# Performance work log

Measured on AMD Instinct MI355X. Metric: run time of the kernel, lower is better.

The kernel has to match this reference:

```python
import jax, jax.numpy as jnp
import numpy as np

NUM_NODES = 20000
NUM_EDGES = 1_000_000
NUM_REL = 12        # internal num_relation (init arg 24 // 2)
NUM_STEP = 6
HID = 128
B_SET = 64          # number of unique (h, r) queries
BS, NEG = 64, 32    # scoring batch
EPS = 1e-10


def setup_inputs() -> dict:
    key = jax.random.key(0)
    ks = jax.random.split(key, 16)
    s = 0.1
    inp = {
        "query_emb": jax.random.normal(ks[0], (2 * NUM_REL + 1, HID), jnp.float32) * s,
        "w_ih": jax.random.normal(ks[1], (4 * HID, HID), jnp.float32) * s,
        "w_hh": jax.random.normal(ks[2], (4 * HID, HID), jnp.float32) * s,
        "b_ih": jax.random.normal(ks[3], (4 * HID,), jnp.float32) * s,
        "b_hh": jax.random.normal(ks[4], (4 * HID,), jnp.float32) * s,
        "wl_w": jax.random.normal(ks[5], (2 * NUM_REL, HID), jnp.float32) * s,
        "wl_b": jax.random.normal(ks[6], (2 * NUM_REL,), jnp.float32) * s,
        "lin_w": jax.random.normal(ks[7], (1, 1), jnp.float32),
        "lin_b": jax.random.normal(ks[8], (1,), jnp.float32),
        "edge_index": jax.random.randint(ks[9], (2, NUM_EDGES), 0, NUM_NODES, jnp.int64),
        "edge_type": jax.random.randint(ks[10], (NUM_EDGES,), 0, 2 * NUM_REL, jnp.int64),
        "h_set": jax.random.randint(ks[11], (B_SET,), 0, NUM_NODES, jnp.int64),
        "r_set": jax.random.randint(ks[12], (B_SET,), 0, NUM_REL, jnp.int64),
        "t_index": jax.random.randint(ks[13], (BS, NEG), 0, NUM_NODES, jnp.int64),
        "hr_inverse": jax.random.randint(ks[14], (BS, NEG), 0, B_SET, jnp.int64),
    }
    return inp


def _lstm(query, w_ih, w_hh, b_ih, b_hh):
    # query: [T, B, D]; single-layer PyTorch LSTM (gate order i, f, g, o)
    B, D = query.shape[1], w_hh.shape[1]
    h0 = jnp.zeros((B, D), query.dtype)

    def step(carry, x):
        h, c = carry
        gates = x @ w_ih.T + b_ih + h @ w_hh.T + b_hh
        i, f, g, o = jnp.split(gates, 4, axis=-1)
        c = jax.nn.sigmoid(f) * c + jax.nn.sigmoid(i) * jnp.tanh(g)
        h = jax.nn.sigmoid(o) * jnp.tanh(c)
        return (h, c), h

    _, hidden = jax.lax.scan(step, (h0, h0), query)
    return hidden  # [T, B, D]


def reference(query_emb, w_ih, w_hh, b_ih, b_hh, wl_w, wl_b, lin_w, lin_b,
              edge_index, edge_type, h_set, r_set, t_index, hr_inverse):
    N1 = NUM_NODES + 1
    B = h_set.shape[0]
    # query sequence: relation repeated (T-1) times, then END token (= NUM_REL)
    q_index = jnp.concatenate(
        [jnp.tile(r_set[None, :], (NUM_STEP - 1, 1)),
         jnp.full((1, B), NUM_REL, dtype=r_set.dtype)], axis=0)  # [T, B]
    query = query_emb[q_index]                                   # [T, B, D]
    hidden = _lstm(query, w_ih, w_hh, b_ih, b_hh)                # [T, B, D]

    memory = jax.nn.one_hot(h_set, N1, dtype=query_emb.dtype)[None]  # [1, B, N1]
    node_in, node_out = edge_index[0], edge_index[1]

    output = None
    for i in range(NUM_STEP):
        k = hidden[i]                 # [B, D]
        v = hidden[: i + 1]           # [i+1, B, D]
        attn = jax.nn.softmax(jnp.einsum('bd,tbd->bt', k, v), axis=-1)
        inp = jnp.einsum('bt,tbn->nb', attn, memory)             # [N1, B]
        weight = jax.nn.softmax(k @ wl_w.T + wl_b, axis=-1).T    # [2R, B]
        # gather -> weight -> scatter_add over edges (edge_weight == 1)
        message = inp[node_in] * weight[edge_type]               # [E, B]
        output = jax.ops.segment_sum(message, node_out, num_segments=N1)
        output = output / jnp.maximum(output.sum(0, keepdims=True), EPS)
        memory = jnp.concatenate([memory, output.T[None]], axis=0)

    score = output[t_index, hr_inverse]           # [BS, NEG]
    return score * lin_w[0, 0] + lin_b[0]
```

## Files before the change

kernel.cpp:

```cpp
#include <hip/hip_runtime.h>
#include <hip/hip_fp16.h>
#include <math.h>

namespace {

constexpr int kN1 = 20001;
constexpr int kNE = 1000000;
constexpr int kNStep = 6;
constexpr int kHid = 128;
constexpr int kB = 64;
constexpr int kNRel2 = 24;
constexpr float kEps = 1e-10f;
constexpr unsigned kSent = (unsigned)kN1;
constexpr int kPMax = kNE + 8 * kN1;
constexpr int kGatherBlocks = 2048;
constexpr int kNWaves = kGatherBlocks * 4;

__device__ __forceinline__ float sig(float x) { return 1.0f / (1.0f + expf(-x)); }

__device__ __forceinline__ float2 cvt2(unsigned u) {
  __half2 h = *reinterpret_cast<__half2*>(&u);
  return __half22float2(h);
}


__global__ __launch_bounds__(256) void transpose_w_kernel(
    const float* __restrict__ w_ih, const float* __restrict__ w_hh,
    float* __restrict__ wt) {
  const int idx = blockIdx.x * 256 + threadIdx.x;
  if (idx < 256 * 512) {
    const int k = idx >> 9;
    const int j = idx & 511;
    wt[idx] = (k < 128) ? w_ih[j * kHid + k] : w_hh[j * kHid + (k - 128)];
  }
}

__global__ __launch_bounds__(512) void lstm_fast_kernel(
    const float* __restrict__ query_emb, const float* __restrict__ wt,
    const float* __restrict__ b_ih, const float* __restrict__ b_hh,
    const int* __restrict__ r_set, float* __restrict__ hidden ) {
  const int b = blockIdx.x;
  const int tid = threadIdx.x;
  __shared__ float xh[256];
  __shared__ float cst[kHid];
  __shared__ float gsm[512];
  const float bias = b_ih[tid] + b_hh[tid];
  const int q = r_set[b];
  if (tid < kHid) { cst[tid] = 0.f; xh[kHid + tid] = 0.f; }
  for (int s = 0; s < kNStep; ++s) {
    if (tid < kHid) xh[tid] = query_emb[((s < kNStep - 1) ? q : 12) * kHid + tid];
    __syncthreads();
    float acc = bias;
#pragma unroll 8
    for (int k = 0; k < 256; ++k) acc += xh[k] * wt[k * 512 + tid];
    gsm[tid] = acc;
    __syncthreads();
    if (tid < kHid) {
      const float ig = sig(gsm[tid]);
      const float fg = sig(gsm[kHid + tid]);
      const float gg = tanhf(gsm[2 * kHid + tid]);
      const float og = sig(gsm[3 * kHid + tid]);
      const float cn = fg * cst[tid] + ig * gg;
      cst[tid] = cn;
      const float hn = og * tanhf(cn);
      xh[kHid + tid] = hn;
      hidden[(s * kB + b) * kHid + tid] = hn;
    }
    __syncthreads();
  }
}

__global__ __launch_bounds__(256) void lstm_kernel(
    const float* __restrict__ query_emb, const float* __restrict__ w_ih,
    const float* __restrict__ w_hh, const float* __restrict__ b_ih,
    const float* __restrict__ b_hh, const int* __restrict__ r_set,
    float* __restrict__ hidden) {
  const int b = blockIdx.x;
  const int tid = threadIdx.x;
  __shared__ float xs[kHid], hs[kHid], cs[kHid], gates[4 * kHid];
  if (tid < kHid) { hs[tid] = 0.f; cs[tid] = 0.f; }
  __syncthreads();
  for (int s = 0; s < kNStep; ++s) {
    const int q = (s < kNStep - 1) ? r_set[b] : 12;
    if (tid < kHid) xs[tid] = query_emb[q * kHid + tid];
    __syncthreads();
    for (int j = tid; j < 4 * kHid; j += blockDim.x) {
      const float* wi = &w_ih[j * kHid];
      const float* wh = &w_hh[j * kHid];
      float a = b_ih[j] + b_hh[j];
#pragma unroll 4
      for (int k = 0; k < kHid; ++k) a += xs[k] * wi[k] + hs[k] * wh[k];
      gates[j] = a;
    }
    __syncthreads();
    if (tid < kHid) {
      const float ig = sig(gates[tid]);
      const float fg = sig(gates[kHid + tid]);
      const float gg = tanhf(gates[2 * kHid + tid]);
      const float og = sig(gates[3 * kHid + tid]);
      const float cn = fg * cs[tid] + ig * gg;
      const float hn = og * tanhf(cn);
      cs[tid] = cn;
      hs[tid] = hn;
      hidden[(s * kB + b) * kHid + tid] = hn;
    }
    __syncthreads();
  }
}

__global__ __launch_bounds__(128) void attn_weight_kernel(
    const float* __restrict__ hidden, const float* __restrict__ wl_w,
    const float* __restrict__ wl_b, float* __restrict__ attnAll ,
    float* __restrict__ weightAll ) {
  const int b = blockIdx.x;
  const int tid = threadIdx.x;
  __shared__ float hsm[kNStep][kHid];
  __shared__ float G[kNStep][kNStep];
  __shared__ float logits[kNStep][kNRel2];
  for (int s = 0; s < kNStep; ++s) hsm[s][tid] = hidden[(s * kB + b) * kHid + tid];
  __syncthreads();
  if (tid < 36) {
    const int i = tid / 6, t = tid % 6;
    if (t <= i) {
      float acc = 0.f;
      for (int k = 0; k < kHid; ++k) acc += hsm[i][k] * hsm[t][k];
      G[i][t] = acc;
    }
  }
  for (int p = tid; p < kNStep * kNRel2; p += 128) {
    const int i = p / kNRel2, r = p % kNRel2;
    float acc = wl_b[r];
    for (int k = 0; k < kHid; ++k) acc += hsm[i][k] * wl_w[r * kHid + k];
    logits[i][r] = acc;
  }
  __syncthreads();
  if (tid < kNStep) {
    const int i = tid;
    float m = G[i][0];
    for (int t = 1; t <= i; ++t) m = fmaxf(m, G[i][t]);
    float ssum = 0.f;
    float ev[kNStep];
    for (int t = 0; t <= i; ++t) { ev[t] = expf(G[i][t] - m); ssum += ev[t]; }
    for (int t = 0; t <= i; ++t) attnAll[(i * kNStep + t) * kB + b] = ev[t] / ssum;
    float mw = logits[i][0];
    for (int r = 1; r < kNRel2; ++r) mw = fmaxf(mw, logits[i][r]);
    float sw = 0.f;
    float ew[kNRel2];
    for (int r = 0; r < kNRel2; ++r) { ew[r] = expf(logits[i][r] - mw); sw += ew[r]; }
    for (int r = 0; r < kNRel2; ++r) weightAll[(i * kNRel2 + r) * kB + b] = ew[r] / sw;
  }
}


__global__ __launch_bounds__(256) void zero_kernel(int* __restrict__ counts,
                                                   float* __restrict__ colsumAll) {
  const int i = blockIdx.x * blockDim.x + threadIdx.x;
  if (i < kN1) counts[i] = 0;
  if (i < kNStep * kB) colsumAll[i] = 0.f;
}

__global__ __launch_bounds__(256) void hist_kernel(const int* __restrict__ nout,
                                                   int* __restrict__ counts) {
  for (int e = blockIdx.x * blockDim.x + threadIdx.x; e < kNE;
       e += gridDim.x * blockDim.x)
    atomicAdd(&counts[nout[e]], 1);
}

__global__ __launch_bounds__(1024) void scan_kernel(const int* __restrict__ counts,
                                                    int* __restrict__ poffsets,
                                                    int* __restrict__ cursor) {
  __shared__ int part[1024];
  const int tid = threadIdx.x;
  const int chunk = (kN1 + 1023) / 1024;
  const int beg = tid * chunk;
  const int end = min(beg + chunk, kN1);
  int s = 0;
  for (int i = beg; i < end; ++i) s += (counts[i] + 7) & ~7;
  part[tid] = s;
  __syncthreads();
  for (int off = 1; off < 1024; off <<= 1) {
    const int v = (tid >= off) ? part[tid - off] : 0;
    __syncthreads();
    part[tid] += v;
    __syncthreads();
  }
  int run = part[tid] - s;
  for (int i = beg; i < end; ++i) {
    poffsets[i] = run;
    cursor[i] = run;
    run += (counts[i] + 7) & ~7;
  }
  if (tid == 1023) poffsets[kN1] = part[1023];
}

__global__ __launch_bounds__(256) void fill_kernel(unsigned* __restrict__ packed) {
  for (int i = blockIdx.x * blockDim.x + threadIdx.x; i < kPMax;
       i += gridDim.x * blockDim.x)
    packed[i] = kSent;
}

__global__ __launch_bounds__(256) void permute_kernel(
    const int* __restrict__ nin, const int* __restrict__ nout,
    const int* __restrict__ etype, int* __restrict__ cursor,
    unsigned* __restrict__ packed) {
  for (int e = blockIdx.x * blockDim.x + threadIdx.x; e < kNE;
       e += gridDim.x * blockDim.x) {
    const int d = nout[e];
    const int pos = atomicAdd(&cursor[d], 1);
    packed[pos] = (unsigned)nin[e] | ((unsigned)etype[e] << 15);
  }
}


__global__ __launch_bounds__(256) void inp_kernel(
    const float* __restrict__ attnAll, const float* __restrict__ colsumAll,
    const int* __restrict__ h_set, const float* __restrict__ outs,
    __half* __restrict__ inp, int step) {
  __shared__ float coef[kNStep][kB];
  __shared__ int hsm[kB];
  const int tid = threadIdx.x;
  for (int j = tid; j < kNStep * kB; j += 256) {
    const int t = j >> 6, b = j & 63;
    float c = 0.f;
    if (t == 0)
      c = attnAll[(step * kNStep) * kB + b];
    else if (t <= step)
      c = attnAll[(step * kNStep + t) * kB + b] /
          fmaxf(colsumAll[(t - 1) * kB + b], kEps);
    coef[t][b] = c;
  }
  if (tid < kB) hsm[tid] = h_set[tid];
  __syncthreads();
  const int total = (kN1 + 1) * 16;
  for (int idx = blockIdx.x * blockDim.x + tid; idx < total;
       idx += gridDim.x * blockDim.x) {
    const int n = idx >> 4;
    const int cg = idx & 15;
    float ax = 0.f, ay = 0.f, az = 0.f, aw = 0.f;
    if (n < kN1) {
      for (int t = 1; t <= step; ++t) {
        const float4 ct = *reinterpret_cast<const float4*>(&coef[t][cg * 4]);
        const float4 o = *reinterpret_cast<const float4*>(
            &outs[((long long)(t - 1) * kN1 + n) * kB + cg * 4]);
        ax += ct.x * o.x; ay += ct.y * o.y; az += ct.z * o.z; aw += ct.w * o.w;
      }
      const int c0 = cg * 4;
      if (hsm[c0 + 0] == n) ax += coef[0][c0 + 0];
      if (hsm[c0 + 1] == n) ay += coef[0][c0 + 1];
      if (hsm[c0 + 2] == n) az += coef[0][c0 + 2];
      if (hsm[c0 + 3] == n) aw += coef[0][c0 + 3];
    }
    __half2 h0 = __floats2half2_rn(ax, ay);
    __half2 h1 = __floats2half2_rn(az, aw);
    uint2 u;
    u.x = *reinterpret_cast<unsigned*>(&h0);
    u.y = *reinterpret_cast<unsigned*>(&h1);
    *reinterpret_cast<uint2*>(inp + (long long)idx * 4) = u;
  }
}

__global__ __launch_bounds__(256) void gather_seg_kernel(
    const __half* __restrict__ inp ,
    const float* __restrict__ weight ,
    const unsigned* __restrict__ packed, const int* __restrict__ poffsets,
    float* __restrict__ out, float* __restrict__ colsum) {
  __shared__ __align__(16) __half wsm[kNRel2 * kB];
  __shared__ float red[4][kB];
  const int tid = threadIdx.x;
  const int lane = tid & 63;
  const int wid = tid >> 6;
  const int g = lane >> 3;
  const int cb = lane & 7;
  for (int j = tid; j < kNRel2 * kB; j += 256) wsm[j] = __float2half(weight[j]);
  __syncthreads();

  float csum[8] = {0.f, 0.f, 0.f, 0.f, 0.f, 0.f, 0.f, 0.f};
  float acc[8] = {0.f, 0.f, 0.f, 0.f, 0.f, 0.f, 0.f, 0.f};

  auto flushNode = [&](int node) {
#pragma unroll
    for (int j = 0; j < 8; ++j) {
      acc[j] += __shfl_xor(acc[j], 8);
      acc[j] += __shfl_xor(acc[j], 16);
      acc[j] += __shfl_xor(acc[j], 32);
    }
    if (g == 0) {
      *reinterpret_cast<float4*>(out + (long long)node * kB + cb * 8) =
          make_float4(acc[0], acc[1], acc[2], acc[3]);
      *reinterpret_cast<float4*>(out + (long long)node * kB + cb * 8 + 4) =
          make_float4(acc[4], acc[5], acc[6], acc[7]);
#pragma unroll
      for (int j = 0; j < 8; ++j) csum[j] += acc[j];
    }
#pragma unroll
    for (int j = 0; j < 8; ++j) acc[j] = 0.f;
  };

  const int wave = blockIdx.x * 4 + wid;
  const int P = poffsets[kN1];
  const int nG = P >> 3;
  const int chunkG = (nG + kNWaves - 1) / kNWaves;
  const int gbeg = wave * chunkG;
  if (gbeg < nG) {
    const int gend = min(gbeg + chunkG, nG);
    auto lb = [&](int x) {
      int lo = 0, hi = kN1;
      while (lo < hi) {
        const int mid = (lo + hi) >> 1;
        if (poffsets[mid] < x) lo = mid + 1; else hi = mid;
      }
      return lo;
    };
    const int nbeg = lb(gbeg * 8);
    const int nend = (gend >= nG) ? kN1 : lb(gend * 8);
    if (nbeg < nend) {
      int n = nbeg;
      int nextB = poffsets[n + 1];
      const int ebeg = poffsets[nbeg];
      const int eend = poffsets[nend];
      unsigned pA = (ebeg < eend) ? packed[ebeg + g] : kSent;
      unsigned pB = (ebeg + 8 < eend) ? packed[ebeg + 8 + g] : kSent;
      uint4 vA = *reinterpret_cast<const uint4*>(
          inp + (long long)(pA & 0x7fffu) * kB + cb * 8);
      uint4 vB = *reinterpret_cast<const uint4*>(
          inp + (long long)(pB & 0x7fffu) * kB + cb * 8);
      for (int ebase = ebeg; ebase < eend; ebase += 16) {
        const bool hasB = (ebase + 8) < eend;
        const int e2 = ebase + 16, e3 = ebase + 24;
        const unsigned pC = (e2 < eend) ? packed[e2 + g] : kSent;
        const unsigned pD = (e3 < eend) ? packed[e3 + g] : kSent;
        while (ebase >= nextB) { flushNode(n); ++n; nextB = poffsets[n + 1]; }
        {
          const uint4 w4 =
              *reinterpret_cast<const uint4*>(wsm + (pA >> 15) * kB + cb * 8);
          const float2 v0 = cvt2(vA.x), v1 = cvt2(vA.y), v2 = cvt2(vA.z), v3 = cvt2(vA.w);
          const float2 w0 = cvt2(w4.x), w1 = cvt2(w4.y), w2 = cvt2(w4.z), w3 = cvt2(w4.w);
          acc[0] += v0.x * w0.x; acc[1] += v0.y * w0.y;
          acc[2] += v1.x * w1.x; acc[3] += v1.y * w1.y;
          acc[4] += v2.x * w2.x; acc[5] += v2.y * w2.y;
          acc[6] += v3.x * w3.x; acc[7] += v3.y * w3.y;
        }
        if (hasB) {
          while (ebase + 8 >= nextB) { flushNode(n); ++n; nextB = poffsets[n + 1]; }
          const uint4 w4 =
              *reinterpret_cast<const uint4*>(wsm + (pB >> 15) * kB + cb * 8);
          const float2 v0 = cvt2(vB.x), v1 = cvt2(vB.y), v2 = cvt2(vB.z), v3 = cvt2(vB.w);
          const float2 w0 = cvt2(w4.x), w1 = cvt2(w4.y), w2 = cvt2(w4.z), w3 = cvt2(w4.w);
          acc[0] += v0.x * w0.x; acc[1] += v0.y * w0.y;
          acc[2] += v1.x * w1.x; acc[3] += v1.y * w1.y;
          acc[4] += v2.x * w2.x; acc[5] += v2.y * w2.y;
          acc[6] += v3.x * w3.x; acc[7] += v3.y * w3.y;
        }
        pA = pC; pB = pD;
        vA = *reinterpret_cast<const uint4*>(
            inp + (long long)(pC & 0x7fffu) * kB + cb * 8);
        vB = *reinterpret_cast<const uint4*>(
            inp + (long long)(pD & 0x7fffu) * kB + cb * 8);
      }
      while (n < nend) { flushNode(n); ++n; }
    }
  }
  if (g == 0) {
#pragma unroll
    for (int j = 0; j < 8; ++j) red[wid][cb * 8 + j] = csum[j];
  }
  __syncthreads();
  if (wid == 0) {
    const float r = red[0][lane] + red[1][lane] + red[2][lane] + red[3][lane];
    unsafeAtomicAdd(&colsum[lane], r);
  }
}

__global__ __launch_bounds__(256) void score_kernel(
    const float* __restrict__ outLast, const float* __restrict__ colsumLast,
    const int* __restrict__ t_index, const int* __restrict__ hr_inverse,
    const float* __restrict__ lin_w, const float* __restrict__ lin_b,
    float* __restrict__ out, int n) {
  const int i = blockIdx.x * blockDim.x + threadIdx.x;
  if (i < n) {
    const int node = t_index[i];
    const int b = hr_inverse[i];
    const float v = outLast[(long long)node * kB + b] / fmaxf(colsumLast[b], kEps);
    out[i] = v * lin_w[0] + lin_b[0];
  }
}


__global__ __launch_bounds__(256) void inp_zero_kernel(
    const float* __restrict__ attnAll, const int* __restrict__ h_set,
    const float* __restrict__ outs, float* __restrict__ inp,
    float* __restrict__ out_next, float* __restrict__ colsum, int step) {
  const long long total = (long long)kN1 * kB;
  for (long long idx = (long long)blockIdx.x * blockDim.x + threadIdx.x; idx < total;
       idx += (long long)gridDim.x * blockDim.x) {
    const int b = (int)(idx & 63);
    const int n = (int)(idx >> 6);
    float acc = (h_set[b] == n) ? attnAll[(step * kNStep) * kB + b] : 0.f;
    for (int t = 1; t <= step; ++t)
      acc += attnAll[(step * kNStep + t) * kB + b] *
             outs[(long long)(t - 1) * kN1 * kB + idx];
    inp[idx] = acc;
    out_next[idx] = 0.f;
  }
  if (blockIdx.x == 0 && threadIdx.x < kB) colsum[threadIdx.x] = 0.f;
}

__global__ __launch_bounds__(256) void scatter_kernel(
    const float* __restrict__ inp, const float* __restrict__ weight,
    const int* __restrict__ nin, const int* __restrict__ nout,
    const int* __restrict__ etype, float* __restrict__ out,
    float* __restrict__ colsum) {
  const int lane = threadIdx.x & 63;
  const int wave = blockIdx.x * (blockDim.x >> 6) + (threadIdx.x >> 6);
  const int nwave = gridDim.x * (blockDim.x >> 6);
  __shared__ float wsm[kNRel2 * kB];
  for (int j = threadIdx.x; j < kNRel2 * kB; j += blockDim.x) wsm[j] = weight[j];
  __syncthreads();
  float csum = 0.f;
  for (int e = wave; e < kNE; e += nwave) {
    const float v = inp[(long long)nin[e] * kB + lane] * wsm[etype[e] * kB + lane];
    unsafeAtomicAdd(&out[(long long)nout[e] * kB + lane], v);
    csum += v;
  }
  unsafeAtomicAdd(&colsum[lane], csum);
}

__global__ __launch_bounds__(256) void normalize_kernel(
    float* __restrict__ out, const float* __restrict__ colsum) {
  const long long total = (long long)kN1 * kB;
  for (long long idx = (long long)blockIdx.x * blockDim.x + threadIdx.x; idx < total;
       idx += (long long)gridDim.x * blockDim.x)
    out[idx] /= fmaxf(colsum[idx & 63], kEps);
}

__global__ __launch_bounds__(256) void score_kernel_norm(
    const float* __restrict__ outLast, const int* __restrict__ t_index,
    const int* __restrict__ hr_inverse, const float* __restrict__ lin_w,
    const float* __restrict__ lin_b, float* __restrict__ out, int n) {
  const int i = blockIdx.x * blockDim.x + threadIdx.x;
  if (i < n) {
    out[i] = outLast[(long long)t_index[i] * kB + hr_inverse[i]] * lin_w[0] + lin_b[0];
  }
}

}

extern "C" void kernel_launch(void* const* d_in, const int* in_sizes, int n_in,
                              void* d_out, int out_size, void* d_ws, size_t ws_size,
                              hipStream_t stream) {
  const float* query_emb = (const float*)d_in[0];
  const float* w_ih = (const float*)d_in[1];
  const float* w_hh = (const float*)d_in[2];
  const float* b_ih = (const float*)d_in[3];
  const float* b_hh = (const float*)d_in[4];
  const float* wl_w = (const float*)d_in[5];
  const float* wl_b = (const float*)d_in[6];
  const float* lin_w = (const float*)d_in[7];
  const float* lin_b = (const float*)d_in[8];
  const int* edge_index = (const int*)d_in[9];
  const int* edge_type = (const int*)d_in[10];
  const int* h_set = (const int*)d_in[11];
  const int* r_set = (const int*)d_in[12];
  const int* t_index = (const int*)d_in[13];
  const int* hr_inverse = (const int*)d_in[14];
  float* out = (float*)d_out;

  const int* nin = edge_index;
  const int* nout = edge_index + kNE;

  float* ws = (float*)d_ws;
  float* hidden = ws;
  float* attnAll = hidden + kNStep * kB * kHid;
  float* weightAll = attnAll + kNStep * kNStep * kB;
  float* colsumAll = weightAll + kNStep * kNRel2 * kB;
  float* inpF32 = colsumAll + kNStep * kB;
  __half* inpH = (__half*)inpF32;
  float* outs = inpF32 + (long long)kN1 * kB;
  float* tail = outs + (long long)kNStep * kN1 * kB;
  int* counts = (int*)tail;
  int* poffsets = counts + kN1;
  int* cursor = poffsets + kN1 + 1;
  unsigned* packed = (unsigned*)(cursor + kN1);
  float* wt = (float*)(packed + kPMax);
  const size_t needed = (size_t)((char*)(wt + 256 * 512) - (char*)d_ws);

  if (ws_size >= needed) {
    transpose_w_kernel<<<512, 256, 0, stream>>>(w_ih, w_hh, wt);
    lstm_fast_kernel<<<kB, 512, 0, stream>>>(query_emb, wt, b_ih, b_hh, r_set, hidden);
    attn_weight_kernel<<<kB, 128, 0, stream>>>(hidden, wl_w, wl_b, attnAll, weightAll);

    zero_kernel<<<(kN1 + 255) / 256, 256, 0, stream>>>(counts, colsumAll);
    hist_kernel<<<1024, 256, 0, stream>>>(nout, counts);
    scan_kernel<<<1, 1024, 0, stream>>>(counts, poffsets, cursor);
    fill_kernel<<<1024, 256, 0, stream>>>(packed);
    permute_kernel<<<1024, 256, 0, stream>>>(nin, nout, edge_type, cursor, packed);

    const int inp_threads = (kN1 + 1) * 16;
    for (int i = 0; i < kNStep; ++i) {
      float* out_i = outs + (long long)i * kN1 * kB;
      inp_kernel<<<(inp_threads + 255) / 256, 256, 0, stream>>>(
          attnAll, colsumAll, h_set, outs, inpH, i);
      gather_seg_kernel<<<kGatherBlocks, 256, 0, stream>>>(
          inpH, weightAll + i * kNRel2 * kB, packed, poffsets, out_i,
          colsumAll + i * kB);
    }
    score_kernel<<<(out_size + 255) / 256, 256, 0, stream>>>(
        outs + 5LL * kN1 * kB, colsumAll + 5 * kB, t_index, hr_inverse, lin_w, lin_b,
        out, out_size);
  } else {
    lstm_kernel<<<kB, 256, 0, stream>>>(query_emb, w_ih, w_hh, b_ih, b_hh, r_set,
                                        hidden);
    attn_weight_kernel<<<kB, 128, 0, stream>>>(hidden, wl_w, wl_b, attnAll, weightAll);
    float* colsum = colsumAll;
    for (int i = 0; i < kNStep; ++i) {
      float* out_i = outs + (long long)i * kN1 * kB;
      inp_zero_kernel<<<2048, 256, 0, stream>>>(attnAll, h_set, outs, inpF32, out_i,
                                                colsum, i);
      scatter_kernel<<<4096, 256, 0, stream>>>(inpF32, weightAll + i * kNRel2 * kB,
                                               nin, nout, edge_type, out_i, colsum);
      normalize_kernel<<<2048, 256, 0, stream>>>(out_i, colsum);
    }
    score_kernel_norm<<<(out_size + 255) / 256, 256, 0, stream>>>(
        outs + 5LL * kN1 * kB, t_index, hr_inverse, lin_w, lin_b, out, out_size);
  }
}
```

Baseline: 669.7 us.

## Replace destination-sorted CSR gather with partitioned source-sorted atomic scatter

Edges are no longer sorted by destination node. They are bucketed into 8 destination partitions and sorted by source inside each partition, using per-XCD histograms and a three-kernel multi-block scan. The step kernel now scatters with float atomics into the output, reusing the source's inp value across consecutive edges. Zeroing of the next output is folded into the inp kernel. This removes the single-block scan, the padding fill and the per-node segment handling, but adds atomic contention on outputs and an extra memory pass. It also stores the count arrays in the outs buffer region, relying on that space being free during preprocessing.

```diff
diff --git a/kernel.cpp b/kernel.cpp
--- a/kernel.cpp
+++ b/kernel.cpp
@@ -4,6 +4,7 @@
 
 namespace {
 
+constexpr int kNN = 20000;
 constexpr int kN1 = 20001;
 constexpr int kNE = 1000000;
 constexpr int kNStep = 6;
@@ -11,17 +12,15 @@
 constexpr int kB = 64;
 constexpr int kNRel2 = 24;
 constexpr float kEps = 1e-10f;
-constexpr unsigned kSent = (unsigned)kN1;
-constexpr int kPMax = kNE + 8 * kN1;
-constexpr int kGatherBlocks = 2048;
-constexpr int kNWaves = kGatherBlocks * 4;
+constexpr int kNXcd = 8;
+constexpr int kPart = 8;
+constexpr int kPSize = 2500;
+constexpr int kKeys = kPart * kNN;
+constexpr int kScanBlocks = (kKeys + 255) / 256;
+
+typedef float f32x4 __attribute__((ext_vector_type(4)));
 
 __device__ __forceinline__ float sig(float x) { return 1.0f / (1.0f + expf(-x)); }
-
-__device__ __forceinline__ float2 cvt2(unsigned u) {
-  __half2 h = *reinterpret_cast<__half2*>(&u);
-  return __half22float2(h);
-}
 
 
 __global__ __launch_bounds__(256) void transpose_w_kernel(
@@ -152,70 +151,121 @@
 }
 
 
-__global__ __launch_bounds__(256) void zero_kernel(int* __restrict__ counts,
-                                                   float* __restrict__ colsumAll) {
-  const int i = blockIdx.x * blockDim.x + threadIdx.x;
-  if (i < kN1) counts[i] = 0;
-  if (i < kNStep * kB) colsumAll[i] = 0.f;
-}
-
-__global__ __launch_bounds__(256) void hist_kernel(const int* __restrict__ nout,
-                                                   int* __restrict__ counts) {
+
+__global__ __launch_bounds__(256) void zero3_kernel(int* __restrict__ count3,
+                                                    float* __restrict__ colsumAll) {
+  const int total = kNXcd * kPart * kNN;
+  for (int i = blockIdx.x * blockDim.x + threadIdx.x; i < total;
+       i += gridDim.x * blockDim.x)
+    count3[i] = 0;
+  if (blockIdx.x == 0 && threadIdx.x < kNStep * kB) colsumAll[threadIdx.x] = 0.f;
+}
+
+__global__ __launch_bounds__(256) void hist3_kernel(const int* __restrict__ nin,
+                                                    const int* __restrict__ nout,
+                                                    int* __restrict__ count3) {
+  const int x = blockIdx.x & (kNXcd - 1);
   for (int e = blockIdx.x * blockDim.x + threadIdx.x; e < kNE;
-       e += gridDim.x * blockDim.x)
-    atomicAdd(&counts[nout[e]], 1);
-}
-
-__global__ __launch_bounds__(1024) void scan_kernel(const int* __restrict__ counts,
-                                                    int* __restrict__ poffsets,
-                                                    int* __restrict__ cursor) {
-  __shared__ int part[1024];
-  const int tid = threadIdx.x;
-  const int chunk = (kN1 + 1023) / 1024;
-  const int beg = tid * chunk;
-  const int end = min(beg + chunk, kN1);
-  int s = 0;
-  for (int i = beg; i < end; ++i) s += (counts[i] + 7) & ~7;
-  part[tid] = s;
+       e += gridDim.x * blockDim.x) {
+    const int p = nout[e] / kPSize;
+    atomicAdd(&count3[(x * kPart + p) * kNN + nin[e]], 1);
+  }
+}
+
+__global__ __launch_bounds__(256) void scanA_kernel(const int* __restrict__ count3,
+                                                    int* __restrict__ blockSum) {
+  const int tid = threadIdx.x;
+  const int kidx = blockIdx.x * 256 + tid;
+  int tot = 0;
+  if (kidx < kKeys) {
+    const int p = kidx / kNN;
+    const int s = kidx - p * kNN;
+#pragma unroll
+    for (int x = 0; x < kNXcd; ++x) tot += count3[(x * kPart + p) * kNN + s];
+  }
+  __shared__ int sm[256];
+  sm[tid] = tot;
+  __syncthreads();
+  for (int off = 128; off > 0; off >>= 1) {
+    if (tid < off) sm[tid] += sm[tid + off];
+    __syncthreads();
+  }
+  if (tid == 0) blockSum[blockIdx.x] = sm[0];
+}
+
+__global__ __launch_bounds__(1024) void scanB_kernel(int* __restrict__ blockSum,
+                                                     int* __restrict__ pOff) {
+  const int tid = threadIdx.x;
+  __shared__ int sm[1024];
+  const int v = (tid < kScanBlocks) ? blockSum[tid] : 0;
+  sm[tid] = v;
   __syncthreads();
   for (int off = 1; off < 1024; off <<= 1) {
-    const int v = (tid >= off) ? part[tid - off] : 0;
-    __syncthreads();
-    part[tid] += v;
-    __syncthreads();
-  }
-  int run = part[tid] - s;
-  for (int i = beg; i < end; ++i) {
-    poffsets[i] = run;
-    cursor[i] = run;
-    run += (counts[i] + 7) & ~7;
-  }
-  if (tid == 1023) poffsets[kN1] = part[1023];
-}
-
-__global__ __launch_bounds__(256) void fill_kernel(unsigned* __restrict__ packed) {
-  for (int i = blockIdx.x * blockDim.x + threadIdx.x; i < kPMax;
-       i += gridDim.x * blockDim.x)
-    packed[i] = kSent;
-}
-
-__global__ __launch_bounds__(256) void permute_kernel(
+    const int t = (tid >= off) ? sm[tid - off] : 0;
+    __syncthreads();
+    sm[tid] += t;
+    __syncthreads();
+  }
+  if (tid < kScanBlocks) blockSum[tid] = sm[tid] - v;
+  if (tid == 0) pOff[kPart] = kNE;
+}
+
+__global__ __launch_bounds__(256) void scanC_kernel(int* __restrict__ count3,
+                                                    const int* __restrict__ blockSum,
+                                                    int* __restrict__ pOff) {
+  const int tid = threadIdx.x;
+  const int kidx = blockIdx.x * 256 + tid;
+  int tot = 0;
+  int p = 0, s = 0;
+  if (kidx < kKeys) {
+    p = kidx / kNN;
+    s = kidx - p * kNN;
+#pragma unroll
+    for (int x = 0; x < kNXcd; ++x) tot += count3[(x * kPart + p) * kNN + s];
+  }
+  __shared__ int sm[256];
+  sm[tid] = tot;
+  __syncthreads();
+  for (int off = 1; off < 256; off <<= 1) {
+    const int t = (tid >= off) ? sm[tid - off] : 0;
+    __syncthreads();
+    sm[tid] += t;
+    __syncthreads();
+  }
+  if (kidx < kKeys) {
+    int sub = sm[tid] - tot + blockSum[blockIdx.x];
+    if (s == 0) pOff[p] = sub;
+#pragma unroll
+    for (int x = 0; x < kNXcd; ++x) {
+      const int idx3 = (x * kPart + p) * kNN + s;
+      const int c = count3[idx3];
+      count3[idx3] = sub;
+      sub += c;
+    }
+  }
+}
+
+__global__ __launch_bounds__(256) void permute3_kernel(
     const int* __restrict__ nin, const int* __restrict__ nout,
-    const int* __restrict__ etype, int* __restrict__ cursor,
+    const int* __restrict__ etype, int* __restrict__ count3,
     unsigned* __restrict__ packed) {
+  const int x = blockIdx.x & (kNXcd - 1);
   for (int e = blockIdx.x * blockDim.x + threadIdx.x; e < kNE;
        e += gridDim.x * blockDim.x) {
     const int d = nout[e];
-    const int pos = atomicAdd(&cursor[d], 1);
-    packed[pos] = (unsigned)nin[e] | ((unsigned)etype[e] << 15);
-  }
-}
-
-
-__global__ __launch_bounds__(256) void inp_kernel(
+    const int p = d / kPSize;
+    const int s = nin[e];
+    const int pos = atomicAdd(&count3[(x * kPart + p) * kNN + s], 1);
+    packed[pos] = (unsigned)s | ((unsigned)etype[e] << 15) |
+                  ((unsigned)(d - p * kPSize) << 20);
+  }
+}
+
+
+__global__ __launch_bounds__(256) void inp_half_zero_kernel(
     const float* __restrict__ attnAll, const float* __restrict__ colsumAll,
     const int* __restrict__ h_set, const float* __restrict__ outs,
-    __half* __restrict__ inp, int step) {
+    __half* __restrict__ inp, float* __restrict__ out_next, int step) {
   __shared__ float coef[kNStep][kB];
   __shared__ int hsm[kB];
   const int tid = threadIdx.x;
@@ -231,139 +281,70 @@
   }
   if (tid < kB) hsm[tid] = h_set[tid];
   __syncthreads();
-  const int total = (kN1 + 1) * 16;
+  const int total = kN1 * 16;
   for (int idx = blockIdx.x * blockDim.x + tid; idx < total;
        idx += gridDim.x * blockDim.x) {
     const int n = idx >> 4;
     const int cg = idx & 15;
     float ax = 0.f, ay = 0.f, az = 0.f, aw = 0.f;
-    if (n < kN1) {
-      for (int t = 1; t <= step; ++t) {
-        const float4 ct = *reinterpret_cast<const float4*>(&coef[t][cg * 4]);
-        const float4 o = *reinterpret_cast<const float4*>(
-            &outs[((long long)(t - 1) * kN1 + n) * kB + cg * 4]);
-        ax += ct.x * o.x; ay += ct.y * o.y; az += ct.z * o.z; aw += ct.w * o.w;
-      }
-      const int c0 = cg * 4;
-      if (hsm[c0 + 0] == n) ax += coef[0][c0 + 0];
-      if (hsm[c0 + 1] == n) ay += coef[0][c0 + 1];
-      if (hsm[c0 + 2] == n) az += coef[0][c0 + 2];
-      if (hsm[c0 + 3] == n) aw += coef[0][c0 + 3];
-    }
+    for (int t = 1; t <= step; ++t) {
+      const float4 ct = *reinterpret_cast<const float4*>(&coef[t][cg * 4]);
+      const f32x4 o = __builtin_nontemporal_load(reinterpret_cast<const f32x4*>(
+          &outs[((long long)(t - 1) * kN1 + n) * kB + cg * 4]));
+      ax += ct.x * o.x; ay += ct.y * o.y; az += ct.z * o.z; aw += ct.w * o.w;
+    }
+    const int c0 = cg * 4;
+    if (hsm[c0 + 0] == n) ax += coef[0][c0 + 0];
+    if (hsm[c0 + 1] == n) ay += coef[0][c0 + 1];
+    if (hsm[c0 + 2] == n) az += coef[0][c0 + 2];
+    if (hsm[c0 + 3] == n) aw += coef[0][c0 + 3];
     __half2 h0 = __floats2half2_rn(ax, ay);
     __half2 h1 = __floats2half2_rn(az, aw);
     uint2 u;
     u.x = *reinterpret_cast<unsigned*>(&h0);
     u.y = *reinterpret_cast<unsigned*>(&h1);
     *reinterpret_cast<uint2*>(inp + (long long)idx * 4) = u;
-  }
-}
-
-__global__ __launch_bounds__(256) void gather_seg_kernel(
-    const __half* __restrict__ inp ,
-    const float* __restrict__ weight ,
-    const unsigned* __restrict__ packed, const int* __restrict__ poffsets,
+    const f32x4 z = {0.f, 0.f, 0.f, 0.f};
+    *reinterpret_cast<f32x4*>(out_next + (long long)idx * 4) = z;
+  }
+}
+
+__global__ __launch_bounds__(256) void scatter_part_kernel(
+    const __half* __restrict__ inpH, const float* __restrict__ weight ,
+    const unsigned* __restrict__ packed, const int* __restrict__ pOff,
     float* __restrict__ out, float* __restrict__ colsum) {
-  __shared__ __align__(16) __half wsm[kNRel2 * kB];
+  __shared__ float wsm[kNRel2 * kB];
   __shared__ float red[4][kB];
   const int tid = threadIdx.x;
   const int lane = tid & 63;
   const int wid = tid >> 6;
-  const int g = lane >> 3;
-  const int cb = lane & 7;
-  for (int j = tid; j < kNRel2 * kB; j += 256) wsm[j] = __float2half(weight[j]);
-  __syncthreads();
-
-  float csum[8] = {0.f, 0.f, 0.f, 0.f, 0.f, 0.f, 0.f, 0.f};
-  float acc[8] = {0.f, 0.f, 0.f, 0.f, 0.f, 0.f, 0.f, 0.f};
-
-  auto flushNode = [&](int node) {
-#pragma unroll
-    for (int j = 0; j < 8; ++j) {
-      acc[j] += __shfl_xor(acc[j], 8);
-      acc[j] += __shfl_xor(acc[j], 16);
-      acc[j] += __shfl_xor(acc[j], 32);
-    }
-    if (g == 0) {
-      *reinterpret_cast<float4*>(out + (long long)node * kB + cb * 8) =
-          make_float4(acc[0], acc[1], acc[2], acc[3]);
-      *reinterpret_cast<float4*>(out + (long long)node * kB + cb * 8 + 4) =
-          make_float4(acc[4], acc[5], acc[6], acc[7]);
-#pragma unroll
-      for (int j = 0; j < 8; ++j) csum[j] += acc[j];
-    }
-#pragma unroll
-    for (int j = 0; j < 8; ++j) acc[j] = 0.f;
-  };
-
-  const int wave = blockIdx.x * 4 + wid;
-  const int P = poffsets[kN1];
-  const int nG = P >> 3;
-  const int chunkG = (nG + kNWaves - 1) / kNWaves;
-  const int gbeg = wave * chunkG;
-  if (gbeg < nG) {
-    const int gend = min(gbeg + chunkG, nG);
-    auto lb = [&](int x) {
-      int lo = 0, hi = kN1;
-      while (lo < hi) {
-        const int mid = (lo + hi) >> 1;
-        if (poffsets[mid] < x) lo = mid + 1; else hi = mid;
-      }
-      return lo;
-    };
-    const int nbeg = lb(gbeg * 8);
-    const int nend = (gend >= nG) ? kN1 : lb(gend * 8);
-    if (nbeg < nend) {
-      int n = nbeg;
-      int nextB = poffsets[n + 1];
-      const int ebeg = poffsets[nbeg];
-      const int eend = poffsets[nend];
-      unsigned pA = (ebeg < eend) ? packed[ebeg + g] : kSent;
-      unsigned pB = (ebeg + 8 < eend) ? packed[ebeg + 8 + g] : kSent;
-      uint4 vA = *reinterpret_cast<const uint4*>(
-          inp + (long long)(pA & 0x7fffu) * kB + cb * 8);
-      uint4 vB = *reinterpret_cast<const uint4*>(
-          inp + (long long)(pB & 0x7fffu) * kB + cb * 8);
-      for (int ebase = ebeg; ebase < eend; ebase += 16) {
-        const bool hasB = (ebase + 8) < eend;
-        const int e2 = ebase + 16, e3 = ebase + 24;
-        const unsigned pC = (e2 < eend) ? packed[e2 + g] : kSent;
-        const unsigned pD = (e3 < eend) ? packed[e3 + g] : kSent;
-        while (ebase >= nextB) { flushNode(n); ++n; nextB = poffsets[n + 1]; }
-        {
-          const uint4 w4 =
-              *reinterpret_cast<const uint4*>(wsm + (pA >> 15) * kB + cb * 8);
-          const float2 v0 = cvt2(vA.x), v1 = cvt2(vA.y), v2 = cvt2(vA.z), v3 = cvt2(vA.w);
-          const float2 w0 = cvt2(w4.x), w1 = cvt2(w4.y), w2 = cvt2(w4.z), w3 = cvt2(w4.w);
-          acc[0] += v0.x * w0.x; acc[1] += v0.y * w0.y;
-          acc[2] += v1.x * w1.x; acc[3] += v1.y * w1.y;
-          acc[4] += v2.x * w2.x; acc[5] += v2.y * w2.y;
-          acc[6] += v3.x * w3.x; acc[7] += v3.y * w3.y;
-        }
-        if (hasB) {
-          while (ebase + 8 >= nextB) { flushNode(n); ++n; nextB = poffsets[n + 1]; }
-          const uint4 w4 =
-              *reinterpret_cast<const uint4*>(wsm + (pB >> 15) * kB + cb * 8);
-          const float2 v0 = cvt2(vB.x), v1 = cvt2(vB.y), v2 = cvt2(vB.z), v3 = cvt2(vB.w);
-          const float2 w0 = cvt2(w4.x), w1 = cvt2(w4.y), w2 = cvt2(w4.z), w3 = cvt2(w4.w);
-          acc[0] += v0.x * w0.x; acc[1] += v0.y * w0.y;
-          acc[2] += v1.x * w1.x; acc[3] += v1.y * w1.y;
-          acc[4] += v2.x * w2.x; acc[5] += v2.y * w2.y;
-          acc[6] += v3.x * w3.x; acc[7] += v3.y * w3.y;
-        }
-        pA = pC; pB = pD;
-        vA = *reinterpret_cast<const uint4*>(
-            inp + (long long)(pC & 0x7fffu) * kB + cb * 8);
-        vB = *reinterpret_cast<const uint4*>(
-            inp + (long long)(pD & 0x7fffu) * kB + cb * 8);
-      }
-      while (n < nend) { flushNode(n); ++n; }
-    }
-  }
-  if (g == 0) {
-#pragma unroll
-    for (int j = 0; j < 8; ++j) red[wid][cb * 8 + j] = csum[j];
-  }
+  for (int j = tid; j < kNRel2 * kB; j += 256) wsm[j] = weight[j];
+  __syncthreads();
+  const int p = blockIdx.x & (kPart - 1);
+  const int v = blockIdx.x >> 3;
+  const int wv = v * 4 + wid;
+  const int ebeg = pOff[p];
+  const int eend = pOff[p + 1];
+  const int cnt = eend - ebeg;
+  const int len = (cnt + 1023) >> 10;
+  const int s0 = ebeg + wv * len;
+  const int s1 = min(s0 + len, eend);
+  const int outBase = p * kPSize * kB;
+  float csum = 0.f;
+  int curSrc = -1;
+  float inv = 0.f;
+  for (int e = s0; e < s1; ++e) {
+    const unsigned u = packed[e];
+    const int src = (int)(u & 0x7fffu);
+    if (src != curSrc) {
+      curSrc = src;
+      inv = __half2float(inpH[src * kB + lane]);
+    }
+    const float vw = inv * wsm[((u >> 15) & 31u) * kB + lane];
+    unsafeAtomicAdd(&out[outBase + (int)(u >> 20) * kB + lane], vw);
+    csum += vw;
+  }
+  red[wid][lane] = csum;
   __syncthreads();
   if (wid == 0) {
     const float r = red[0][lane] + red[1][lane] + red[2][lane] + red[3][lane];
@@ -473,15 +454,15 @@
   float* attnAll = hidden + kNStep * kB * kHid;
   float* weightAll = attnAll + kNStep * kNStep * kB;
   float* colsumAll = weightAll + kNStep * kNRel2 * kB;
-  float* inpF32 = colsumAll + kNStep * kB;
-  __half* inpH = (__half*)inpF32;
-  float* outs = inpF32 + (long long)kN1 * kB;
+  float* inpRegion = colsumAll + kNStep * kB;
+  __half* inpH = (__half*)inpRegion;
+  float* outs = inpRegion + (long long)kN1 * kB;
+  int* count3 = (int*)(outs + 5LL * kN1 * kB);
   float* tail = outs + (long long)kNStep * kN1 * kB;
-  int* counts = (int*)tail;
-  int* poffsets = counts + kN1;
-  int* cursor = poffsets + kN1 + 1;
-  unsigned* packed = (unsigned*)(cursor + kN1);
-  float* wt = (float*)(packed + kPMax);
+  int* blockSum = (int*)tail;
+  int* pOff = blockSum + 1024;
+  unsigned* packed = (unsigned*)(pOff + 16);
+  float* wt = (float*)(packed + kNE);
   const size_t needed = (size_t)((char*)(wt + 256 * 512) - (char*)d_ws);
 
   if (ws_size >= needed) {
@@ -489,25 +470,27 @@
     lstm_fast_kernel<<<kB, 512, 0, stream>>>(query_emb, wt, b_ih, b_hh, r_set, hidden);
     attn_weight_kernel<<<kB, 128, 0, stream>>>(hidden, wl_w, wl_b, attnAll, weightAll);
 
-    zero_kernel<<<(kN1 + 255) / 256, 256, 0, stream>>>(counts, colsumAll);
-    hist_kernel<<<1024, 256, 0, stream>>>(nout, counts);
-    scan_kernel<<<1, 1024, 0, stream>>>(counts, poffsets, cursor);
-    fill_kernel<<<1024, 256, 0, stream>>>(packed);
-    permute_kernel<<<1024, 256, 0, stream>>>(nin, nout, edge_type, cursor, packed);
-
-    const int inp_threads = (kN1 + 1) * 16;
+    zero3_kernel<<<2048, 256, 0, stream>>>(count3, colsumAll);
+    hist3_kernel<<<1024, 256, 0, stream>>>(nin, nout, count3);
+    scanA_kernel<<<kScanBlocks, 256, 0, stream>>>(count3, blockSum);
+    scanB_kernel<<<1, 1024, 0, stream>>>(blockSum, pOff);
+    scanC_kernel<<<kScanBlocks, 256, 0, stream>>>(count3, blockSum, pOff);
+    permute3_kernel<<<1024, 256, 0, stream>>>(nin, nout, edge_type, count3, packed);
+
     for (int i = 0; i < kNStep; ++i) {
       float* out_i = outs + (long long)i * kN1 * kB;
-      inp_kernel<<<(inp_threads + 255) / 256, 256, 0, stream>>>(
-          attnAll, colsumAll, h_set, outs, inpH, i);
-      gather_seg_kernel<<<kGatherBlocks, 256, 0, stream>>>(
-          inpH, weightAll + i * kNRel2 * kB, packed, poffsets, out_i,
-          colsumAll + i * kB);
+      inp_half_zero_kernel<<<1280, 256, 0, stream>>>(attnAll, colsumAll, h_set, outs,
+                                                     inpH, out_i, i);
+      scatter_part_kernel<<<2048, 256, 0, stream>>>(inpH,
+                                                    weightAll + i * kNRel2 * kB,
+                                                    packed, pOff, out_i,
+                                                    colsumAll + i * kB);
     }
     score_kernel<<<(out_size + 255) / 256, 256, 0, stream>>>(
         outs + 5LL * kN1 * kB, colsumAll + 5 * kB, t_index, hr_inverse, lin_w, lin_b,
         out, out_size);
   } else {
+    float* inpF32 = inpRegion;
     lstm_kernel<<<kB, 256, 0, stream>>>(query_emb, w_ih, w_hh, b_ih, b_hh, r_set,
                                         hidden);
     attn_weight_kernel<<<kB, 128, 0, stream>>>(hidden, wl_w, wl_b, attnAll, weightAll);
```

New measurement: 1.748 ms. 161% more time.
